# Performance work log

Hardware: AMD Instinct MI355X
Metric: run time of the kernel (lower is better)

Reference implementation:

```python
import jax, jax.numpy as jnp
import numpy as np

B, L, D = 2048, 64, 128
NODES = 512
EPS = 1e-6


def setup_inputs() -> dict:
    key = jax.random.key(0)
    ks = jax.random.split(key, 9)
    src_ids = jax.random.randint(ks[0], (B, L), 0, NODES, dtype=jnp.int32)
    dst_ids = jax.random.randint(ks[1], (B, L), 0, NODES, dtype=jnp.int32)
    src_node_ids = jax.random.randint(ks[2], (B,), 1, NODES, dtype=jnp.int32)
    dst_node_ids = jax.random.randint(ks[3], (B,), 1, NODES, dtype=jnp.int32)
    node_interact_times = 100.0 + jax.random.uniform(ks[4], (B,), jnp.float32)
    src_times = jax.random.uniform(ks[5], (B, L), jnp.float32) * 100.0
    dst_times = jax.random.uniform(ks[6], (B, L), jnp.float32) * 100.0
    W1 = jax.random.normal(ks[7], (1, D), jnp.float32) * 0.5
    b1 = jnp.zeros((D,), jnp.float32)
    W2 = jax.random.normal(ks[8], (D, D), jnp.float32) * (1.0 / np.sqrt(D))
    b2 = jnp.zeros((D,), jnp.float32)
    return dict(src_padded_nodes_neighbor_ids=src_ids,
                dst_padded_nodes_neighbor_ids=dst_ids,
                src_node_ids=src_node_ids, dst_node_ids=dst_node_ids,
                node_interact_times=node_interact_times,
                src_padded_nodes_neighbor_times=src_times,
                dst_padded_nodes_neighbor_times=dst_times,
                W1=W1, b1=b1, W2=W2, b2=b2)


def _group_stats(ids, t):
    # per-position stats of the group sharing the same neighbor id. ids,t: (L,)
    n_pos = ids.shape[0]
    eq = ids[:, None] == ids[None, :]                       # (L,L) group membership
    n = eq.sum(1)                                           # group size at each position
    nf = n.astype(t.dtype)
    tb = jnp.broadcast_to(t[None, :], (n_pos, n_pos))
    tmax = jnp.max(jnp.where(eq, tb, -jnp.inf), axis=1)
    tmin = jnp.min(jnp.where(eq, tb, jnp.inf), axis=1)
    # mean(diff(sorted(ts))) == (max-min)/(n-1)
    avg_iat = jnp.where(n > 1, (tmax - tmin) / jnp.maximum(nf - 1.0, 1.0), 0.0)
    # stable rank of each element inside its own group (order statistic)
    pos = jnp.arange(n_pos)
    before = (t[:, None] < t[None, :]) | ((t[:, None] == t[None, :]) & (pos[:, None] < pos[None, :]))
    rank = jnp.sum(eq & before, axis=0)
    split = n // 2
    sel = eq & (rank[None, :] == split[:, None])            # exactly one per group
    t_split = jnp.sum(jnp.where(sel, tb, 0.0), axis=1)      # sorted(ts)[n//2]
    denom = jnp.maximum(nf - split.astype(t.dtype) - 1.0, 1.0)
    recent_iat = jnp.where(n >= 4, (tmax - t_split) / denom, 0.0)
    valid = ids != 0                                        # dicts skip neighbor id 0
    return nf, jnp.where(valid, avg_iat, 0.0), jnp.where(valid, recent_iat, 0.0)


def _cross_lookup(ids_a, ids_b, vals_b):
    # dict.get(nid, 0.0) over the other side's per-group values (id 0 excluded)
    match = (ids_a[:, None] == ids_b[None, :]) & (ids_b[None, :] != 0)
    idx = jnp.argmax(match, axis=1)
    return jnp.where(match.any(1), vals_b[idx], 0.0)


def _last_time(ids_a, ids_b, t_b):
    # dict comprehension keeps the LAST occurrence's timestamp (id 0 excluded)
    match = (ids_a[:, None] == ids_b[None, :]) & (ids_b[None, :] != 0)
    score = jnp.where(match, jnp.arange(ids_b.shape[0])[None, :], -1)
    li = score.max(1)
    return jnp.where(li >= 0, t_b[jnp.maximum(li, 0)], 0.0)


def _side_features(ids_a, t_a, ids_b, t_b, other_node_id, cur_t,
                   n_a, avg_a, rec_a, avg_b, rec_b, other_first):
    ft = t_a.dtype
    c_self = n_a
    c_other = jnp.sum(ids_a[:, None] == ids_b[None, :], axis=1).astype(ft)
    is_other = (ids_a == other_node_id).astype(ft)
    connects = (c_other > 0).astype(ft)
    freq_asym = jnp.where(c_other > 0, c_self / (c_other + EPS), 0.0)
    rcy_self = cur_t - t_a
    rcy_other = cur_t - _last_time(ids_a, ids_b, t_b)
    temp_asym = jnp.where(rcy_self > EPS, rcy_other / (rcy_self + EPS), 0.0)
    iat_other = _cross_lookup(ids_a, ids_b, avg_b)
    iat_asym = jnp.where(iat_other > EPS, avg_a / (iat_other + EPS), 0.0)
    riat_other = _cross_lookup(ids_a, ids_b, rec_b)
    riat_asym = jnp.where(riat_other > EPS, rec_a / (riat_other + EPS), 0.0)
    if other_first:
        head = [c_other, c_self]
    else:
        head = [c_self, c_other]
    return jnp.stack(head + [is_other, connects, freq_asym, temp_asym, iat_asym, riat_asym], axis=1)


def _per_sample(ids_s, ids_d, sid, did, cur_t, t_s, t_d):
    n_s, avg_s, rec_s = _group_stats(ids_s, t_s)
    n_d, avg_d, rec_d = _group_stats(ids_d, t_d)
    f_src = _side_features(ids_s, t_s, ids_d, t_d, did, cur_t,
                           n_s, avg_s, rec_s, avg_d, rec_d, False)
    f_dst = _side_features(ids_d, t_d, ids_s, t_s, sid, cur_t,
                           n_d, avg_d, rec_d, avg_s, rec_s, True)
    return f_src, f_dst


def _mlp_sum(feats, W1, b1, W2, b2):
    # Linear(1->D) -> ReLU -> Linear(D->D), applied per scalar feature, summed over the 8 features
    h = jax.nn.relu(feats[..., None] * W1[0] + b1)           # [B,L,8,D]
    y = jnp.einsum('blfd,de->blfe', h, W2) + b2
    return y.sum(axis=2)                                      # [B,L,D]


def reference(src_padded_nodes_neighbor_ids, dst_padded_nodes_neighbor_ids,
              src_node_ids, dst_node_ids, node_interact_times,
              src_padded_nodes_neighbor_times, dst_padded_nodes_neighbor_times,
              W1, b1, W2, b2):
    f_src, f_dst = jax.vmap(_per_sample)(
        src_padded_nodes_neighbor_ids, dst_padded_nodes_neighbor_ids,
        src_node_ids, dst_node_ids, node_interact_times,
        src_padded_nodes_neighbor_times, dst_padded_nodes_neighbor_times)
    f_src = jnp.where((src_padded_nodes_neighbor_ids == 0)[..., None], 0.0, f_src)
    f_dst = jnp.where((dst_padded_nodes_neighbor_ids == 0)[..., None], 0.0, f_dst)
    src_path_features = _mlp_sum(f_src, W1, b1, W2, b2)
    dst_path_features = _mlp_sum(f_dst, W1, b1, W2, b2)
    return src_path_features, dst_path_features
```

## Files before the change

kernel.cpp:

```cpp
#include <hip/hip_runtime.h>


#define EPSF 1e-6f
#define LDB 136

typedef __attribute__((ext_vector_type(8))) short bf16x8;
typedef __attribute__((ext_vector_type(4))) float f32x4;

__device__ inline short f2bf(float x) {
    unsigned u = __float_as_uint(x);
    return (short)((u + 0x7fffu + ((u >> 16) & 1u)) >> 16);
}

__global__ void w2t_prep(const float* __restrict__ W2, short* __restrict__ w2t) {
    const int idx = blockIdx.x * 256 + threadIdx.x;
    const int k = idx >> 7, n = idx & 127;
    w2t[n * 128 + k] = f2bf(W2[idx]);
}

template <bool FROMWS>
__launch_bounds__(256, 3)
__global__ void lpe_fused2(const int* __restrict__ src_ids,
                           const int* __restrict__ dst_ids,
                           const int* __restrict__ src_nid,
                           const int* __restrict__ dst_nid,
                           const float* __restrict__ t_now,
                           const float* __restrict__ src_t,
                           const float* __restrict__ dst_t,
                           const float* __restrict__ W1,
                           const float* __restrict__ b1,
                           const float* __restrict__ W2,
                           const float* __restrict__ b2,
                           const short* __restrict__ w2t,
                           float* __restrict__ out)
{
    __shared__ int2  s_idt[256];
    __shared__ float s_nt[4][512];
    __shared__ float s_avgt[4][512];
    __shared__ float s_rect[4][512];
    __shared__ float s_lastt[4][512];
    __shared__ float s_feats[256][9];
    __shared__ float s_w1[128], s_b1[128];
    __shared__ short W2T[FROMWS ? 8 : 128 * LDB];

    const int tid   = threadIdx.x;
    const int r     = tid;
    const int h     = r >> 7;
    const int b     = blockIdx.x * 2 + h;
    const int side  = (r >> 6) & 1;
    const int i     = r & 63;
    const int ss    = r >> 6;
    const int sbase = r & ~63;

    #pragma unroll
    for (int u = tid; u < 2048; u += 256) ((float*)s_nt)[u] = 0.f;

    const int*   idp = side ? dst_ids : src_ids;
    const float* tp  = side ? dst_t   : src_t;
    const int   my_id = idp[b * 64 + i];
    const float my_t  = tp[b * 64 + i];
    s_idt[r] = make_int2(my_id, __float_as_int(my_t));
    if (tid < 128) { s_w1[tid] = W1[tid]; s_b1[tid] = b1[tid]; }
    if constexpr (!FROMWS) {
        for (int u = tid; u < 16384; u += 256) {
            const int k = u >> 7, n = u & 127;
            W2T[n * LDB + k] = f2bf(W2[u]);
        }
    }
    __syncthreads();

    int n = 0, rank = 0, later = 0;
    float tmax = -3.4e38f, tmin = 3.4e38f;
    #pragma unroll 8
    for (int j = 0; j < 64; ++j) {
        const int2 e = s_idt[sbase + j];
        const float tj = __int_as_float(e.y);
        if (e.x == my_id) {
            ++n;
            tmax = fmaxf(tmax, tj);
            tmin = fminf(tmin, tj);
            if (tj < my_t || (tj == my_t && j < i)) ++rank;
            if (j > i) later = 1;
        }
    }
    const float nf    = (float)n;
    const int   split = n >> 1;
    const float avg   = (n > 1) ? (tmax - tmin) / (nf - 1.f) : 0.f;
    if (my_id != 0) {
        s_nt[ss][my_id]   = nf;
        s_avgt[ss][my_id] = avg;
        if (rank == split)
            s_rect[ss][my_id] = (n >= 4)
                ? (tmax - my_t) / fmaxf(nf - (float)split - 1.f, 1.f) : 0.f;
        if (!later)
            s_lastt[ss][my_id] = my_t;
    }
    __syncthreads();

    {
        const int   os    = ss ^ 1;
        const float avg_m = (my_id != 0) ? avg : 0.f;
        const float rec_m = (my_id != 0) ? s_rect[ss][my_id] : 0.f;
        const float n_o   = (my_id != 0) ? s_nt[os][my_id] : 0.f;
        const bool  hit   = n_o > 0.f;
        const float avg_o = hit ? s_avgt[os][my_id] : 0.f;
        const float rec_o = hit ? s_rect[os][my_id] : 0.f;
        const float lastt = hit ? s_lastt[os][my_id] : 0.f;
        const float cur   = t_now[b];
        const int other_node = side ? src_nid[b] : dst_nid[b];
        const float m = (my_id != 0) ? 1.f : 0.f;

        const float rcy_s = cur - my_t;
        const float rcy_o = cur - lastt;
        s_feats[r][0] = m * nf;
        s_feats[r][1] = m * n_o;
        s_feats[r][2] = m * ((my_id == other_node) ? 1.f : 0.f);
        s_feats[r][3] = m * (hit ? 1.f : 0.f);
        s_feats[r][4] = m * (hit ? nf / (n_o + EPSF) : 0.f);
        s_feats[r][5] = m * ((rcy_s > EPSF) ? rcy_o / (rcy_s + EPSF) : 0.f);
        s_feats[r][6] = m * ((avg_o > EPSF) ? avg_m / (avg_o + EPSF) : 0.f);
        s_feats[r][7] = m * ((rec_o > EPSF) ? rec_m / (rec_o + EPSF) : 0.f);
    }
    __syncthreads();

    const int lane = tid & 63, wv = tid >> 6;
    const int quad = lane >> 4, ln = lane & 15;

    float fxr[4][8];
    #pragma unroll
    for (int rg = 0; rg < 4; ++rg) {
        const int row = wv * 64 + rg * 16 + ln;
        #pragma unroll
        for (int j = 0; j < 8; ++j) fxr[rg][j] = s_feats[row][j];
    }

    bf16x8 gf[4][4];
    #pragma unroll
    for (int kk = 0; kk < 4; ++kk) {
        const int kb = kk * 32 + quad * 8;
        #pragma unroll
        for (int rg = 0; rg < 4; ++rg) {
            #pragma unroll
            for (int u = 0; u < 8; ++u) {
                const float w  = s_w1[kb + u];
                const float bb = s_b1[kb + u];
                float s = fmaxf(fmaf(fxr[rg][0], w, bb), 0.f);
                s += fmaxf(fmaf(fxr[rg][1], w, bb), 0.f);
                s += fmaxf(fmaf(fxr[rg][2], w, bb), 0.f);
                s += fmaxf(fmaf(fxr[rg][3], w, bb), 0.f);
                s += fmaxf(fmaf(fxr[rg][4], w, bb), 0.f);
                s += fmaxf(fmaf(fxr[rg][5], w, bb), 0.f);
                s += fmaxf(fmaf(fxr[rg][6], w, bb), 0.f);
                s += fmaxf(fmaf(fxr[rg][7], w, bb), 0.f);
                gf[rg][kk][u] = f2bf(s);
            }
        }
    }

    const long side_stride = 2048L * 64L * 128L;
    #pragma unroll
    for (int et = 0; et < 8; ++et) {
        bf16x8 af[4];
        #pragma unroll
        for (int kk = 0; kk < 4; ++kk) {
            if constexpr (FROMWS)
                af[kk] = *(const bf16x8*)&w2t[(et * 16 + ln) * 128 + kk * 32 + quad * 8];
            else
                af[kk] = *(const bf16x8*)&W2T[(et * 16 + ln) * LDB + kk * 32 + quad * 8];
        }
        f32x4 acc[4];
        #pragma unroll
        for (int rg = 0; rg < 4; ++rg) acc[rg] = (f32x4){0.f, 0.f, 0.f, 0.f};
        #pragma unroll
        for (int kk = 0; kk < 4; ++kk)
            #pragma unroll
            for (int rg = 0; rg < 4; ++rg)
                acc[rg] = __builtin_amdgcn_mfma_f32_16x16x32_bf16(af[kk], gf[rg][kk], acc[rg], 0, 0, 0);

        const int e0 = et * 16 + quad * 4;
        const f32x4 badd = *(const f32x4*)&b2[e0] * 8.f;
        #pragma unroll
        for (int rg = 0; rg < 4; ++rg) {
            const int row = wv * 64 + rg * 16 + ln;
            const int h2 = row >> 7, sd = (row >> 6) & 1, ii = row & 63;
            const long bq = (long)blockIdx.x * 2 + h2;
            *(f32x4*)&out[(long)sd * side_stride + (bq * 64 + ii) * 128 + e0]
                = acc[rg] + badd;
        }
    }
}

extern "C" void kernel_launch(void* const* d_in, const int* in_sizes, int n_in,
                              void* d_out, int out_size, void* d_ws, size_t ws_size,
                              hipStream_t stream) {
    (void)in_sizes; (void)n_in; (void)out_size;
    const int*   src_ids = (const int*)  d_in[0];
    const int*   dst_ids = (const int*)  d_in[1];
    const int*   src_nid = (const int*)  d_in[2];
    const int*   dst_nid = (const int*)  d_in[3];
    const float* t_now   = (const float*)d_in[4];
    const float* src_t   = (const float*)d_in[5];
    const float* dst_t   = (const float*)d_in[6];
    const float* W1      = (const float*)d_in[7];
    const float* b1      = (const float*)d_in[8];
    const float* W2      = (const float*)d_in[9];
    const float* b2      = (const float*)d_in[10];
    float* out = (float*)d_out;

    if (ws_size >= (size_t)(128 * 128 * 2)) {
        short* w2t = (short*)d_ws;
        w2t_prep<<<64, 256, 0, stream>>>(W2, w2t);
        lpe_fused2<true><<<1024, 256, 0, stream>>>(src_ids, dst_ids, src_nid, dst_nid,
                                                   t_now, src_t, dst_t, W1, b1, W2, b2,
                                                   w2t, out);
    } else {
        lpe_fused2<false><<<1024, 256, 0, stream>>>(src_ids, dst_ids, src_nid, dst_nid,
                                                    t_now, src_t, dst_t, W1, b1, W2, b2,
                                                    nullptr, out);
    }
}
```

Before: 211.5 us.

## Process one sample per block with packed per-node stat table

Changes the work split from two samples per 256-thread block to one sample per block over twice as many blocks. The four per-node LDS stat arrays are packed into one float4 table, which cuts shared memory and the zeroing work. Each wave now handles 32 MFMA rows instead of 64, which lowers register pressure, and the launch bound is raised to allow 4 blocks per CU. The first-layer ReLU-sum is vectorised into float2 operations. The cost is that half the threads sit idle during the grouping phase, and W2 fragments are reloaded by twice as many blocks.

```diff
diff --git a/kernel.cpp b/kernel.cpp
--- a/kernel.cpp
+++ b/kernel.cpp
@@ -6,6 +6,7 @@
 
 typedef __attribute__((ext_vector_type(8))) short bf16x8;
 typedef __attribute__((ext_vector_type(4))) float f32x4;
+typedef __attribute__((ext_vector_type(2))) float f32x2;
 
 __device__ inline short f2bf(float x) {
     unsigned u = __float_as_uint(x);
@@ -19,8 +20,8 @@
 }
 
 template <bool FROMWS>
-__launch_bounds__(256, 3)
-__global__ void lpe_fused2(const int* __restrict__ src_ids,
+__launch_bounds__(256, 4)
+__global__ void lpe_fused1(const int* __restrict__ src_ids,
                            const int* __restrict__ dst_ids,
                            const int* __restrict__ src_nid,
                            const int* __restrict__ dst_nid,
@@ -34,33 +35,30 @@
                            const short* __restrict__ w2t,
                            float* __restrict__ out)
 {
-    __shared__ int2  s_idt[256];
-    __shared__ float s_nt[4][512];
-    __shared__ float s_avgt[4][512];
-    __shared__ float s_rect[4][512];
-    __shared__ float s_lastt[4][512];
-    __shared__ float s_feats[256][9];
+    __shared__ int2  s_idt[128];
+    __shared__ f32x4 s_tab[2][512];
+    __shared__ float s_feats[128][9];
     __shared__ float s_w1[128], s_b1[128];
     __shared__ short W2T[FROMWS ? 8 : 128 * LDB];
 
-    const int tid   = threadIdx.x;
-    const int r     = tid;
-    const int h     = r >> 7;
-    const int b     = blockIdx.x * 2 + h;
-    const int side  = (r >> 6) & 1;
-    const int i     = r & 63;
-    const int ss    = r >> 6;
-    const int sbase = r & ~63;
-
-    #pragma unroll
-    for (int u = tid; u < 2048; u += 256) ((float*)s_nt)[u] = 0.f;
-
-    const int*   idp = side ? dst_ids : src_ids;
-    const float* tp  = side ? dst_t   : src_t;
-    const int   my_id = idp[b * 64 + i];
-    const float my_t  = tp[b * 64 + i];
-    s_idt[r] = make_int2(my_id, __float_as_int(my_t));
+    const int tid = threadIdx.x;
+    const int b   = blockIdx.x;
+
+    #pragma unroll
+    for (int u = tid; u < 1024; u += 256) ((float*)s_tab)[u * 4] = 0.f;
     if (tid < 128) { s_w1[tid] = W1[tid]; s_b1[tid] = b1[tid]; }
+
+    const int side = (tid >> 6) & 1;
+    const int i    = tid & 63;
+    int   my_id = 0;
+    float my_t  = 0.f;
+    if (tid < 128) {
+        const int*   idp = side ? dst_ids : src_ids;
+        const float* tp  = side ? dst_t   : src_t;
+        my_id = idp[b * 64 + i];
+        my_t  = tp [b * 64 + i];
+        s_idt[tid] = make_int2(my_id, __float_as_int(my_t));
+    }
     if constexpr (!FROMWS) {
         for (int u = tid; u < 16384; u += 256) {
             const int k = u >> 7, n = u & 127;
@@ -69,95 +67,99 @@
     }
     __syncthreads();
 
-    int n = 0, rank = 0, later = 0;
-    float tmax = -3.4e38f, tmin = 3.4e38f;
-    #pragma unroll 8
-    for (int j = 0; j < 64; ++j) {
-        const int2 e = s_idt[sbase + j];
-        const float tj = __int_as_float(e.y);
-        if (e.x == my_id) {
-            ++n;
-            tmax = fmaxf(tmax, tj);
-            tmin = fminf(tmin, tj);
-            if (tj < my_t || (tj == my_t && j < i)) ++rank;
-            if (j > i) later = 1;
-        }
-    }
-    const float nf    = (float)n;
-    const int   split = n >> 1;
-    const float avg   = (n > 1) ? (tmax - tmin) / (nf - 1.f) : 0.f;
-    if (my_id != 0) {
-        s_nt[ss][my_id]   = nf;
-        s_avgt[ss][my_id] = avg;
-        if (rank == split)
-            s_rect[ss][my_id] = (n >= 4)
-                ? (tmax - my_t) / fmaxf(nf - (float)split - 1.f, 1.f) : 0.f;
-        if (!later)
-            s_lastt[ss][my_id] = my_t;
+    float nf = 0.f, avg = 0.f;
+    if (tid < 128) {
+        int n = 0, rank = 0, later = 0;
+        float tmax = -3.4e38f, tmin = 3.4e38f;
+        const int sbase = side * 64;
+        #pragma unroll 8
+        for (int j = 0; j < 64; ++j) {
+            const int2 e = s_idt[sbase + j];
+            const float tj = __int_as_float(e.y);
+            if (e.x == my_id) {
+                ++n;
+                tmax = fmaxf(tmax, tj);
+                tmin = fminf(tmin, tj);
+                if (tj < my_t || (tj == my_t && j < i)) ++rank;
+                if (j > i) later = 1;
+            }
+        }
+        nf = (float)n;
+        const int split = n >> 1;
+        avg = (n > 1) ? (tmax - tmin) / (nf - 1.f) : 0.f;
+        if (my_id != 0) {
+            s_tab[side][my_id].x = nf;
+            s_tab[side][my_id].y = avg;
+            if (rank == split)
+                s_tab[side][my_id].z = (n >= 4)
+                    ? (tmax - my_t) / fmaxf(nf - (float)split - 1.f, 1.f) : 0.f;
+            if (!later)
+                s_tab[side][my_id].w = my_t;
+        }
     }
     __syncthreads();
 
-    {
-        const int   os    = ss ^ 1;
-        const float avg_m = (my_id != 0) ? avg : 0.f;
-        const float rec_m = (my_id != 0) ? s_rect[ss][my_id] : 0.f;
-        const float n_o   = (my_id != 0) ? s_nt[os][my_id] : 0.f;
-        const bool  hit   = n_o > 0.f;
-        const float avg_o = hit ? s_avgt[os][my_id] : 0.f;
-        const float rec_o = hit ? s_rect[os][my_id] : 0.f;
-        const float lastt = hit ? s_lastt[os][my_id] : 0.f;
-        const float cur   = t_now[b];
+    if (tid < 128) {
+        const int os = side ^ 1;
+        const float rec_m = (my_id != 0) ? s_tab[side][my_id].z : 0.f;
+        const f32x4 to = s_tab[os][my_id];
+        const float n_o = (my_id != 0) ? to.x : 0.f;
+        const bool  hit = n_o > 0.f;
+        const float avg_o = hit ? to.y : 0.f;
+        const float rec_o = hit ? to.z : 0.f;
+        const float lastt = hit ? to.w : 0.f;
+        const float cur = t_now[b];
         const int other_node = side ? src_nid[b] : dst_nid[b];
         const float m = (my_id != 0) ? 1.f : 0.f;
 
         const float rcy_s = cur - my_t;
         const float rcy_o = cur - lastt;
-        s_feats[r][0] = m * nf;
-        s_feats[r][1] = m * n_o;
-        s_feats[r][2] = m * ((my_id == other_node) ? 1.f : 0.f);
-        s_feats[r][3] = m * (hit ? 1.f : 0.f);
-        s_feats[r][4] = m * (hit ? nf / (n_o + EPSF) : 0.f);
-        s_feats[r][5] = m * ((rcy_s > EPSF) ? rcy_o / (rcy_s + EPSF) : 0.f);
-        s_feats[r][6] = m * ((avg_o > EPSF) ? avg_m / (avg_o + EPSF) : 0.f);
-        s_feats[r][7] = m * ((rec_o > EPSF) ? rec_m / (rec_o + EPSF) : 0.f);
+        s_feats[tid][0] = m * nf;
+        s_feats[tid][1] = m * n_o;
+        s_feats[tid][2] = m * ((my_id == other_node) ? 1.f : 0.f);
+        s_feats[tid][3] = m * (hit ? 1.f : 0.f);
+        s_feats[tid][4] = m * (hit ? nf / (n_o + EPSF) : 0.f);
+        s_feats[tid][5] = m * ((rcy_s > EPSF) ? rcy_o / (rcy_s + EPSF) : 0.f);
+        s_feats[tid][6] = m * ((avg_o > EPSF) ? avg / (avg_o + EPSF) : 0.f);
+        s_feats[tid][7] = m * ((rec_o > EPSF) ? rec_m / (rec_o + EPSF) : 0.f);
     }
     __syncthreads();
 
     const int lane = tid & 63, wv = tid >> 6;
     const int quad = lane >> 4, ln = lane & 15;
 
-    float fxr[4][8];
-    #pragma unroll
-    for (int rg = 0; rg < 4; ++rg) {
-        const int row = wv * 64 + rg * 16 + ln;
+    float fxr[2][8];
+    #pragma unroll
+    for (int rg = 0; rg < 2; ++rg) {
+        const int row = wv * 32 + rg * 16 + ln;
         #pragma unroll
         for (int j = 0; j < 8; ++j) fxr[rg][j] = s_feats[row][j];
     }
 
-    bf16x8 gf[4][4];
+    bf16x8 gf[2][4];
     #pragma unroll
     for (int kk = 0; kk < 4; ++kk) {
         const int kb = kk * 32 + quad * 8;
         #pragma unroll
-        for (int rg = 0; rg < 4; ++rg) {
+        for (int rg = 0; rg < 2; ++rg) {
             #pragma unroll
-            for (int u = 0; u < 8; ++u) {
-                const float w  = s_w1[kb + u];
-                const float bb = s_b1[kb + u];
-                float s = fmaxf(fmaf(fxr[rg][0], w, bb), 0.f);
-                s += fmaxf(fmaf(fxr[rg][1], w, bb), 0.f);
-                s += fmaxf(fmaf(fxr[rg][2], w, bb), 0.f);
-                s += fmaxf(fmaf(fxr[rg][3], w, bb), 0.f);
-                s += fmaxf(fmaf(fxr[rg][4], w, bb), 0.f);
-                s += fmaxf(fmaf(fxr[rg][5], w, bb), 0.f);
-                s += fmaxf(fmaf(fxr[rg][6], w, bb), 0.f);
-                s += fmaxf(fmaf(fxr[rg][7], w, bb), 0.f);
-                gf[rg][kk][u] = f2bf(s);
+            for (int u2 = 0; u2 < 4; ++u2) {
+                const f32x2 w  = *(const f32x2*)&s_w1[kb + u2 * 2];
+                const f32x2 bb = *(const f32x2*)&s_b1[kb + u2 * 2];
+                f32x2 s = {0.f, 0.f};
+                #pragma unroll
+                for (int f = 0; f < 8; ++f) {
+                    const f32x2 h = w * fxr[rg][f] + bb;
+                    s += __builtin_elementwise_max(h, (f32x2){0.f, 0.f});
+                }
+                gf[rg][kk][u2 * 2]     = f2bf(s.x);
+                gf[rg][kk][u2 * 2 + 1] = f2bf(s.y);
             }
         }
     }
 
     const long side_stride = 2048L * 64L * 128L;
+    const long rowbase = (long)b * 64;
     #pragma unroll
     for (int et = 0; et < 8; ++et) {
         bf16x8 af[4];
@@ -168,23 +170,20 @@
             else
                 af[kk] = *(const bf16x8*)&W2T[(et * 16 + ln) * LDB + kk * 32 + quad * 8];
         }
-        f32x4 acc[4];
-        #pragma unroll
-        for (int rg = 0; rg < 4; ++rg) acc[rg] = (f32x4){0.f, 0.f, 0.f, 0.f};
+        f32x4 acc[2] = {(f32x4){0.f, 0.f, 0.f, 0.f}, (f32x4){0.f, 0.f, 0.f, 0.f}};
         #pragma unroll
         for (int kk = 0; kk < 4; ++kk)
             #pragma unroll
-            for (int rg = 0; rg < 4; ++rg)
+            for (int rg = 0; rg < 2; ++rg)
                 acc[rg] = __builtin_amdgcn_mfma_f32_16x16x32_bf16(af[kk], gf[rg][kk], acc[rg], 0, 0, 0);
 
         const int e0 = et * 16 + quad * 4;
         const f32x4 badd = *(const f32x4*)&b2[e0] * 8.f;
         #pragma unroll
-        for (int rg = 0; rg < 4; ++rg) {
-            const int row = wv * 64 + rg * 16 + ln;
-            const int h2 = row >> 7, sd = (row >> 6) & 1, ii = row & 63;
-            const long bq = (long)blockIdx.x * 2 + h2;
-            *(f32x4*)&out[(long)sd * side_stride + (bq * 64 + ii) * 128 + e0]
+        for (int rg = 0; rg < 2; ++rg) {
+            const int row = wv * 32 + rg * 16 + ln;
+            const int sd = row >> 6, ii = row & 63;
+            *(f32x4*)&out[(long)sd * side_stride + (rowbase + ii) * 128 + e0]
                 = acc[rg] + badd;
         }
     }
@@ -210,11 +209,11 @@
     if (ws_size >= (size_t)(128 * 128 * 2)) {
         short* w2t = (short*)d_ws;
         w2t_prep<<<64, 256, 0, stream>>>(W2, w2t);
-        lpe_fused2<true><<<1024, 256, 0, stream>>>(src_ids, dst_ids, src_nid, dst_nid,
+        lpe_fused1<true><<<2048, 256, 0, stream>>>(src_ids, dst_ids, src_nid, dst_nid,
                                                    t_now, src_t, dst_t, W1, b1, W2, b2,
                                                    w2t, out);
     } else {
-        lpe_fused2<false><<<1024, 256, 0, stream>>>(src_ids, dst_ids, src_nid, dst_nid,
+        lpe_fused1<false><<<2048, 256, 0, stream>>>(src_ids, dst_ids, src_nid, dst_nid,
                                                     t_now, src_t, dst_t, W1, b1, W2, b2,
                                                     nullptr, out);
     }
```

Result: faster. 192.7 us (-8.9%).
